# Optimization experiments

Hardware: AMD Instinct MI355X
Metric: run time of the kernel (lower is better)

The kernel has to match this reference:

```python
import jax, jax.numpy as jnp
import numpy as np

def setup_inputs() -> dict:
    key = jax.random.key(0)
    kS, kD = jax.random.split(key)
    B, Ls, Ld, d = 8, 2048, 2048, 1024
    S = jax.random.normal(kS, (B, Ls, d), dtype=jnp.float32)
    D = jax.random.normal(kD, (B, Ld, d), dtype=jnp.float32)
    return {"S": S, "D": D}

def reference(S, D):
    # scores_D: [B, Ld, Ls] = D @ S^T ; scores_S: [B, Ls, Ld] = S @ D^T
    attn_D = jax.nn.softmax(jnp.einsum('bld,bmd->blm', D, S), axis=-1)
    attn_S = jax.nn.softmax(jnp.einsum('bmd,bld->bml', S, D), axis=-1)
    co_D = D + jnp.einsum('blm,bmd->bld', attn_D, S)
    co_S = S + jnp.einsum('bml,bld->bmd', attn_S, D)
    return (co_D, co_S)
```

## Files before the change

kernel.cpp:

```cpp
#include <hip/hip_runtime.h>

typedef __attribute__((ext_vector_type(8))) _Float16 f16x8;
typedef __attribute__((ext_vector_type(16))) float f32x16;

#define B_    8
#define LSEQ  2048
#define DIM   1024
#define QBLK  64
#define KBLK  128
#define NKB   (LSEQ / KBLK)
#define NBAND 8
#define SHIFT 104.0f

#define TILE_US   16384
#define KIMG_US   ((size_t)2 * 8 * 16 * 8 * TILE_US)
#define WS_NEED   ((size_t)2 * KIMG_US * 2)
#define WS_NEW    ((size_t)3 * KIMG_US * 2)

static __device__ __forceinline__ unsigned pk2(float a, float b) {
    return __builtin_bit_cast(unsigned, __builtin_amdgcn_cvt_pkrtz(a, b));
}

#define VMCNT(n) asm volatile("s_waitcnt vmcnt(" #n ")" ::: "memory")
#define LGKM0()  asm volatile("s_waitcnt lgkmcnt(0)" ::: "memory")
#define BAR()    do { asm volatile("" ::: "memory"); __builtin_amdgcn_s_barrier(); \
                      asm volatile("" ::: "memory"); } while (0)

static __device__ __forceinline__ void gll16(const void* g, void* l) {
    __builtin_amdgcn_global_load_lds(
        (const __attribute__((address_space(1))) void*)g,
        (__attribute__((address_space(3))) void*)l, 16, 0, 0);
}

static __device__ __forceinline__ void issue32(const unsigned short* gt, unsigned short* lb, int w, int lane) {
    #pragma unroll
    for (int j = 0; j < 4; ++j) {
        const int off = (w * 4 + j) * 1024;
        gll16((const char*)gt + off + lane * 16, (char*)lb + off);
    }
}
static __device__ __forceinline__ void issue16(const unsigned short* gt, unsigned short* lb, int w, int lane) {
    #pragma unroll
    for (int j = 0; j < 2; ++j) {
        const int off = (w * 2 + j) * 1024;
        gll16((const char*)gt + off + lane * 16, (char*)lb + off);
    }
}

__global__ __launch_bounds__(256)
void prepass(const float* __restrict__ Sp, const float* __restrict__ Dp,
             unsigned short* __restrict__ Kimg, unsigned short* __restrict__ Vimg)
{
    const int blk = blockIdx.x;
    const int dc = blk & 7;
    const int kb = (blk >> 3) & 15;
    const int b  = (blk >> 7) & 7;
    const int m  = blk >> 10;
    const float* src = (m ? Dp : Sp) + ((size_t)b * LSEQ + kb * 128) * DIM + dc * 128;
    unsigned short* kt = Kimg + (size_t)((((m * 8 + b) * 16 + kb) * 8) + dc) * TILE_US;
    unsigned short* vt = Vimg + (size_t)((((m * 8 + b) * 8 + dc) * 16) + kb) * TILE_US;

    __shared__ unsigned short tile[128 * 132];
    const int t = threadIdx.x;

    #pragma unroll
    for (int i = 0; i < 16; ++i) {
        const int idx = t + i * 256;
        const int r = idx >> 5;
        const int c4 = (idx & 31) << 2;
        const float4 v = *(const float4*)(src + (size_t)r * DIM + c4);
        const unsigned lo = pk2(v.x, v.y), hi2 = pk2(v.z, v.w);
        *(uint2*)(kt + r * 128 + (c4 ^ ((r & 15) << 3))) = make_uint2(lo, hi2);
        *(uint2*)(&tile[r * 132 + c4]) = make_uint2(lo, hi2);
    }
    __syncthreads();
    #pragma unroll
    for (int i = 0; i < 32; ++i) {
        const int widx = t + i * 256;
        const int dcl = widx >> 6;
        const int wk  = widx & 63;
        const unsigned a  = tile[(wk * 2) * 132 + dcl];
        const unsigned bb = tile[(wk * 2 + 1) * 132 + dcl];
        ((unsigned*)vt)[dcl * 64 + (wk ^ ((dcl & 15) << 2))] = a | (bb << 16);
    }
}

__global__ __launch_bounds__(512, 2)
void coattn_qk(const unsigned short* __restrict__ Kimg,
               unsigned short* __restrict__ scores)
{
    const int s  = blockIdx.x;
    const int b  = s & 7;
    const int qb = s >> 3;
    const int q0 = qb * QBLK;

    const unsigned short* kbase = Kimg + (size_t)(0 * 8 + b) * 16 * 8 * TILE_US;
    const unsigned short* qbase = Kimg + (size_t)(1 * 8 + b) * 16 * 8 * TILE_US
                                + (size_t)(qb >> 1) * 8 * TILE_US + (size_t)(qb & 1) * 8192;
    unsigned short* scb = scores + (size_t)b * LSEQ * LSEQ;

    __shared__ unsigned short Rr[3][16384];
    __shared__ unsigned short QR_[3][8192];

    const int t    = threadIdx.x;
    const int lane = t & 63;
    const int w    = t >> 6;
    const int l31  = lane & 31;
    const int hi   = lane >> 5;
    const int ksub = w & 3;
    const int qh   = w >> 2;

    const int krow = ksub * 32 + l31;
    const int qrow = qh * 32 + l31;
    const int kswz = (krow & 15) << 3;
    const int qswz = (qrow & 15) << 3;

    #define QK_MMA(SLOT)                                                          \
    do {                                                                          \
        const unsigned short* Kb = Rr[SLOT];                                      \
        const unsigned short* Qb = QR_[SLOT];                                     \
        __builtin_amdgcn_s_setprio(1);                                            \
        _Pragma("unroll")                                                         \
        for (int kc = 0; kc < 8; ++kc) {                                          \
            const int d0 = kc * 16 + hi * 8;                                      \
            f16x8 a  = *(const f16x8*)&Kb[krow * 128 + (d0 ^ kswz)];              \
            f16x8 bq = *(const f16x8*)&Qb[qrow * 128 + (d0 ^ qswz)];              \
            C = __builtin_amdgcn_mfma_f32_32x32x16_f16(a, bq, C, 0, 0, 0);        \
        }                                                                         \
        __builtin_amdgcn_s_setprio(0);                                            \
    } while (0)

    #pragma unroll 1
    for (int kb = 0; kb < NKB; ++kb) {
        const unsigned short* kt = kbase + (size_t)kb * 8 * TILE_US;

        f32x16 C;
        #pragma unroll
        for (int r = 0; r < 16; ++r) C[r] = 0.0f;

        BAR();
        issue32(kt + 0 * TILE_US, Rr[0], w, lane);
        issue16(qbase + 0 * TILE_US, QR_[0], w, lane);
        issue32(kt + 1 * TILE_US, Rr[1], w, lane);
        issue16(qbase + 1 * TILE_US, QR_[1], w, lane);
        VMCNT(6);
        BAR();

        issue32(kt + 2 * TILE_US, Rr[2], w, lane);
        issue16(qbase + 2 * TILE_US, QR_[2], w, lane);
        VMCNT(6);
        QK_MMA(0);

        BAR();
        issue32(kt + 3 * TILE_US, Rr[0], w, lane);
        issue16(qbase + 3 * TILE_US, QR_[0], w, lane);
        VMCNT(6);
        QK_MMA(1);

        BAR();
        issue32(kt + 4 * TILE_US, Rr[1], w, lane);
        issue16(qbase + 4 * TILE_US, QR_[1], w, lane);
        VMCNT(6);
        QK_MMA(2);

        BAR();
        issue32(kt + 5 * TILE_US, Rr[2], w, lane);
        issue16(qbase + 5 * TILE_US, QR_[2], w, lane);
        VMCNT(6);
        QK_MMA(0);

        BAR();
        issue32(kt + 6 * TILE_US, Rr[0], w, lane);
        issue16(qbase + 6 * TILE_US, QR_[0], w, lane);
        VMCNT(6);
        QK_MMA(1);

        BAR();
        issue32(kt + 7 * TILE_US, Rr[1], w, lane);
        issue16(qbase + 7 * TILE_US, QR_[1], w, lane);
        VMCNT(6);
        QK_MMA(2);

        BAR();
        VMCNT(0);
        QK_MMA(0);

        BAR();
        QK_MMA(1);

        {
            const size_t rowoff = (size_t)(q0 + 32 * qh + l31) * LSEQ + kb * 128 + 32 * ksub;
            #pragma unroll
            for (int rp = 0; rp < 8; ++rp) {
                const int r  = rp * 2;
                const int kk = (r & 3) + 8 * (r >> 2) + 4 * hi;
                *(unsigned*)(scb + rowoff + kk) = pk2(C[r] - SHIFT, C[r + 1] - SHIFT);
            }
        }
    }
}

__global__ __launch_bounds__(512, 2)
void coattn_pv(const float* __restrict__ Sp, const float* __restrict__ Dp,
               float* __restrict__ outp,
               const unsigned short* __restrict__ Vimg,
               const unsigned short* __restrict__ scores,
               const int trans)
{
    const int s  = blockIdx.x;
    const int b  = s & 7;
    const int qb = s >> 3;
    const int q0 = qb * QBLK;

    const float* Qg = (trans ? Sp : Dp) + (size_t)b * LSEQ * DIM;
    float* Og = outp + (size_t)(trans ? 1 : 0) * ((size_t)B_ * LSEQ * DIM) + (size_t)b * LSEQ * DIM;
    const unsigned short* vbase = Vimg + (size_t)((trans ? 1 : 0) * 8 + b) * 8 * 16 * TILE_US;
    const unsigned short* scb = scores + (size_t)b * LSEQ * LSEQ;

    __shared__ unsigned short Rr[3][16384];
    __shared__ unsigned short Pst[QBLK * 128];
    __shared__ float alf[QBLK];

    const int t    = threadIdx.x;
    const int lane = t & 63;
    const int w    = t >> 6;
    const int l31  = lane & 31;
    const int hi   = lane >> 5;
    const int ksub = w & 3;
    const int qh   = w >> 2;

    const int qrow = qh * 32 + l31;
    const int qswz = (qrow & 15);
    const int dcl  = ksub * 32 + l31;
    const int vswz = (dcl & 15) << 3;

    const int srow = t >> 3;
    const int soct = t & 7;

    f32x16 O[NBAND];
    #pragma unroll
    for (int i = 0; i < NBAND; ++i)
        #pragma unroll
        for (int r = 0; r < 16; ++r) O[i][r] = 0.0f;

    float m_run = -INFINITY, l_run = 0.0f;

    #define PV_MMA(BAND, SLOT)                                                    \
    do {                                                                          \
        const unsigned short* Vb = Rr[SLOT];                                      \
        __builtin_amdgcn_s_setprio(1);                                            \
        _Pragma("unroll")                                                         \
        for (int kc = 0; kc < 8; ++kc) {                                          \
            const int kk0 = kc * 16 + hi * 8;                                     \
            f16x8 vb = *(const f16x8*)&Vb[dcl * 128 + (kk0 ^ vswz)];              \
            O[BAND] = __builtin_amdgcn_mfma_f32_32x32x16_f16(pa[kc], vb, O[BAND], 0, 0, 0); \
        }                                                                         \
        __builtin_amdgcn_s_setprio(0);                                            \
    } while (0)

    #define ISSUE_V(VI, SL) issue32(vbase + (size_t)((VI) * 16 + kb) * TILE_US, Rr[SL], w, lane)

    #pragma unroll 1
    for (int kb = 0; kb < NKB; ++kb) {
        BAR();

        if (!trans) {
            #pragma unroll
            for (int j = 0; j < 2; ++j) {
                const int G = (w * 2 + j) * 64 + lane;
                const int qq = G >> 4, gg = G & 15;
                const unsigned short* src = scb + (size_t)(q0 + qq) * LSEQ + kb * 128
                                          + ((gg ^ (qq & 15)) << 3);
                gll16(src, (char*)Pst + G * 16);
            }
        }
        ISSUE_V(0, 0);
        ISSUE_V(1, 1);
        if (!trans) { VMCNT(8); }
        BAR();

        if (trans) {
            const int drp = t >> 3;
            const int oct = t & 7;
            const unsigned short* s0 = scb + (size_t)(kb * 128 + 2 * drp) * LSEQ + q0 + oct * 8;
            const uint4 a  = *(const uint4*)s0;
            const uint4 bb = *(const uint4*)(s0 + LSEQ);
            const unsigned short* au = (const unsigned short*)&a;
            const unsigned short* bu = (const unsigned short*)&bb;
            #pragma unroll
            for (int i = 0; i < 8; ++i) {
                const int sc = oct * 8 + i;
                const unsigned v = (unsigned)au[i] | ((unsigned)bu[i] << 16);
                *(unsigned*)((char*)Pst + sc * 256 + ((((drp >> 2) ^ (sc & 15)) << 4) + (drp & 3) * 4)) = v;
            }
            LGKM0(); BAR();
        }

        {
            const int g0 = soct * 2;
            char* a0 = (char*)Pst + srow * 256 + (((g0    ) ^ (srow & 15)) << 4);
            char* a1 = (char*)Pst + srow * 256 + (((g0 + 1) ^ (srow & 15)) << 4);
            f16x8 v0 = *(const f16x8*)a0;
            f16x8 v1 = *(const f16x8*)a1;
            float sv[16];
            #pragma unroll
            for (int i = 0; i < 8; ++i) { sv[i] = (float)v0[i]; sv[8 + i] = (float)v1[i]; }
            float rm = sv[0];
            #pragma unroll
            for (int i = 1; i < 16; ++i) rm = fmaxf(rm, sv[i]);
            rm = fmaxf(rm, __shfl_xor(rm, 1));
            rm = fmaxf(rm, __shfl_xor(rm, 2));
            rm = fmaxf(rm, __shfl_xor(rm, 4));
            const float mn = fmaxf(m_run, rm);
            const float al = __expf(m_run - mn);
            float ps = 0.0f;
            #pragma unroll
            for (int i = 0; i < 16; ++i) { sv[i] = __expf(sv[i] - mn); ps += sv[i]; }
            ps += __shfl_xor(ps, 1);
            ps += __shfl_xor(ps, 2);
            ps += __shfl_xor(ps, 4);
            l_run = l_run * al + ps;
            m_run = mn;
            uint4 o0, o1;
            o0.x = pk2(sv[0], sv[1]);  o0.y = pk2(sv[2], sv[3]);
            o0.z = pk2(sv[4], sv[5]);  o0.w = pk2(sv[6], sv[7]);
            o1.x = pk2(sv[8], sv[9]);  o1.y = pk2(sv[10], sv[11]);
            o1.z = pk2(sv[12], sv[13]); o1.w = pk2(sv[14], sv[15]);
            *(uint4*)a0 = o0;
            *(uint4*)a1 = o1;
            if (soct == 0) alf[srow] = al;
        }
        LGKM0(); VMCNT(4); BAR();

        f16x8 pa[8];
        #pragma unroll
        for (int kc = 0; kc < 8; ++kc)
            pa[kc] = *(const f16x8*)((char*)Pst + qrow * 256 + (((2 * kc + hi) ^ qswz) << 4));
        {
            float alr[16];
            #pragma unroll
            for (int r = 0; r < 16; ++r)
                alr[r] = alf[qh * 32 + (r & 3) + 8 * (r >> 2) + 4 * hi];
            #pragma unroll
            for (int i = 0; i < NBAND; ++i)
                #pragma unroll
                for (int r = 0; r < 16; ++r) O[i][r] *= alr[r];
        }

        ISSUE_V(2, 2); VMCNT(4); PV_MMA(0, 0); BAR();
        ISSUE_V(3, 0); VMCNT(4); PV_MMA(1, 1); BAR();
        ISSUE_V(4, 1); VMCNT(4); PV_MMA(2, 2); BAR();
        ISSUE_V(5, 2); VMCNT(4); PV_MMA(3, 0); BAR();
        ISSUE_V(6, 0); VMCNT(4); PV_MMA(4, 1); BAR();
        ISSUE_V(7, 1); VMCNT(4); PV_MMA(5, 2); BAR();
        VMCNT(0);      PV_MMA(6, 0); BAR();
        PV_MMA(7, 1);
    }

    __syncthreads();
    if (soct == 0) alf[srow] = 1.0f / l_run;
    __syncthreads();
    #pragma unroll
    for (int r = 0; r < 16; ++r) {
        const int qr = qh * 32 + (r & 3) + 8 * (r >> 2) + 4 * hi;
        const float il = alf[qr];
        const size_t rowoff = (size_t)(q0 + qr) * DIM;
        #pragma unroll
        for (int band = 0; band < NBAND; ++band) {
            const int dcol = band * 128 + ksub * 32 + l31;
            Og[rowoff + dcol] = Qg[rowoff + dcol] + O[band][r] * il;
        }
    }
    #undef PV_MMA
    #undef ISSUE_V
    #undef QK_MMA
}

__global__ __launch_bounds__(512, 2)
void coattn_main(const float* __restrict__ Sp, const float* __restrict__ Dp,
                 float* __restrict__ outp,
                 const unsigned short* __restrict__ Kimg,
                 const unsigned short* __restrict__ Vimg)
{
    const int s   = blockIdx.x;
    const int g   = (s & 7) | ((s >> 8) << 3);
    const int qb  = (s >> 3) & 31;
    const int dir = g >> 3;
    const int b   = g & 7;
    const int mat_k = dir;
    const int mat_q = 1 - dir;

    const float* Qg = (dir ? Sp : Dp) + (size_t)b * LSEQ * DIM;
    float* Og = outp + (size_t)dir * ((size_t)B_ * LSEQ * DIM) + (size_t)b * LSEQ * DIM;
    const int q0 = qb * QBLK;

    const unsigned short* kbase = Kimg + (size_t)(mat_k * 8 + b) * 16 * 8 * TILE_US;
    const unsigned short* qbase = Kimg + (size_t)(mat_q * 8 + b) * 16 * 8 * TILE_US
                                + (size_t)(qb >> 1) * 8 * TILE_US + (size_t)(qb & 1) * 8192;
    const unsigned short* vbase = Vimg + (size_t)(mat_k * 8 + b) * 8 * 16 * TILE_US;

    __shared__ unsigned short Rr[3][16384];
    __shared__ unsigned short QR_[3][8192];
    __shared__ float redmax[2][4][32];
    __shared__ float redsum[2][4][32];
    __shared__ float alf[QBLK];

    const int t    = threadIdx.x;
    const int lane = t & 63;
    const int w    = t >> 6;
    const int l31  = lane & 31;
    const int hi   = lane >> 5;
    const int ksub = w & 3;
    const int qh   = w >> 2;

    const int krow = ksub * 32 + l31;
    const int qrow = qh * 32 + l31;
    const int kswz = (krow & 15) << 3;
    const int qswz = (qrow & 15) << 3;
    const int dcl  = ksub * 32 + l31;
    const int vswz = (dcl & 15) << 3;

    unsigned short* Plds = QR_[0];

    f32x16 O[NBAND];
    #pragma unroll
    for (int i = 0; i < NBAND; ++i)
        #pragma unroll
        for (int r = 0; r < 16; ++r) O[i][r] = 0.0f;

    float m_run = -INFINITY, l_run = 0.0f;

    #define QK_MMA(SLOT)                                                          \
    do {                                                                          \
        const unsigned short* Kb = Rr[SLOT];                                      \
        const unsigned short* Qb = QR_[SLOT];                                     \
        __builtin_amdgcn_s_setprio(1);                                            \
        _Pragma("unroll")                                                         \
        for (int kc = 0; kc < 8; ++kc) {                                          \
            const int d0 = kc * 16 + hi * 8;                                      \
            f16x8 a  = *(const f16x8*)&Kb[krow * 128 + (d0 ^ kswz)];              \
            f16x8 bq = *(const f16x8*)&Qb[qrow * 128 + (d0 ^ qswz)];              \
            C = __builtin_amdgcn_mfma_f32_32x32x16_f16(a, bq, C, 0, 0, 0);        \
        }                                                                         \
        __builtin_amdgcn_s_setprio(0);                                            \
    } while (0)

    #define PV_MMA(BAND, SLOT)                                                    \
    do {                                                                          \
        const unsigned short* Vb = Rr[SLOT];                                      \
        __builtin_amdgcn_s_setprio(1);                                            \
        _Pragma("unroll")                                                         \
        for (int kc = 0; kc < 8; ++kc) {                                          \
            const int kk0 = kc * 16 + hi * 8;                                     \
            f16x8 vb = *(const f16x8*)&Vb[dcl * 128 + (kk0 ^ vswz)];              \
            O[BAND] = __builtin_amdgcn_mfma_f32_32x32x16_f16(pa[kc], vb, O[BAND], 0, 0, 0); \
        }                                                                         \
        __builtin_amdgcn_s_setprio(0);                                            \
    } while (0)

    #pragma unroll 1
    for (int kb = 0; kb < NKB; ++kb) {
        const unsigned short* kt = kbase + (size_t)kb * 8 * TILE_US;

        f32x16 C;
        #pragma unroll
        for (int r = 0; r < 16; ++r) C[r] = 0.0f;

        BAR();
        issue32(kt + 0 * TILE_US, Rr[0], w, lane);
        issue16(qbase + 0 * TILE_US, QR_[0], w, lane);
        issue32(kt + 1 * TILE_US, Rr[1], w, lane);
        issue16(qbase + 1 * TILE_US, QR_[1], w, lane);
        VMCNT(6);
        BAR();

        issue32(kt + 2 * TILE_US, Rr[2], w, lane);
        issue16(qbase + 2 * TILE_US, QR_[2], w, lane);
        VMCNT(6);
        QK_MMA(0);

        BAR();
        issue32(kt + 3 * TILE_US, Rr[0], w, lane);
        issue16(qbase + 3 * TILE_US, QR_[0], w, lane);
        VMCNT(6);
        QK_MMA(1);

        BAR();
        issue32(kt + 4 * TILE_US, Rr[1], w, lane);
        issue16(qbase + 4 * TILE_US, QR_[1], w, lane);
        VMCNT(6);
        QK_MMA(2);

        BAR();
        issue32(kt + 5 * TILE_US, Rr[2], w, lane);
        issue16(qbase + 5 * TILE_US, QR_[2], w, lane);
        VMCNT(6);
        QK_MMA(0);

        BAR();
        issue32(kt + 6 * TILE_US, Rr[0], w, lane);
        issue16(qbase + 6 * TILE_US, QR_[0], w, lane);
        VMCNT(6);
        QK_MMA(1);

        BAR();
        issue32(kt + 7 * TILE_US, Rr[1], w, lane);
        issue16(qbase + 7 * TILE_US, QR_[1], w, lane);
        VMCNT(6);
        QK_MMA(2);

        BAR();
        issue32(vbase + (size_t)(0 * 16 + kb) * TILE_US, Rr[2], w, lane);
        VMCNT(4);
        QK_MMA(0);

        BAR();
        issue32(vbase + (size_t)(1 * 16 + kb) * TILE_US, Rr[0], w, lane);
        VMCNT(4);
        QK_MMA(1);

        float rm = -INFINITY;
        #pragma unroll
        for (int r = 0; r < 16; ++r) rm = fmaxf(rm, C[r]);
        rm = fmaxf(rm, __shfl_xor(rm, 32));
        if (lane < 32) redmax[qh][ksub][l31] = rm;
        __syncthreads();

        const float bm = fmaxf(fmaxf(redmax[qh][0][l31], redmax[qh][1][l31]),
                               fmaxf(redmax[qh][2][l31], redmax[qh][3][l31]));
        const float mn = fmaxf(m_run, bm);
        const float al = __expf(m_run - mn);
        float p[16];
        float ps = 0.0f;
        #pragma unroll
        for (int r = 0; r < 16; ++r) { p[r] = __expf(C[r] - mn); ps += p[r]; }
        ps += __shfl_xor(ps, 32);
        if (lane < 32) {
            redsum[qh][ksub][l31] = ps;
            if (ksub == 0) alf[qh * 32 + l31] = al;
        }
        {
            #pragma unroll
            for (int rp = 0; rp < 8; ++rp) {
                const int r  = rp * 2;
                const int kk = ksub * 32 + (r & 3) + 8 * (r >> 2) + 4 * hi;
                *(unsigned*)&Plds[qrow * KBLK + (kk ^ qswz)] = pk2(p[r], p[r + 1]);
            }
        }
        __syncthreads();

        const float bs = redsum[qh][0][l31] + redsum[qh][1][l31] +
                         redsum[qh][2][l31] + redsum[qh][3][l31];
        l_run = l_run * al + bs;
        m_run = mn;

        float alr[16];
        #pragma unroll
        for (int r = 0; r < 16; ++r)
            alr[r] = alf[qh * 32 + (r & 3) + 8 * (r >> 2) + 4 * hi];
        #pragma unroll
        for (int i = 0; i < NBAND; ++i)
            #pragma unroll
            for (int r = 0; r < 16; ++r) O[i][r] *= alr[r];

        f16x8 pa[8];
        #pragma unroll
        for (int kc = 0; kc < 8; ++kc) {
            const int kk0 = kc * 16 + hi * 8;
            pa[kc] = *(const f16x8*)&Plds[qrow * KBLK + (kk0 ^ qswz)];
        }

        issue32(vbase + (size_t)(2 * 16 + kb) * TILE_US, Rr[1], w, lane);
        VMCNT(4);
        PV_MMA(0, 2);

        BAR();
        issue32(vbase + (size_t)(3 * 16 + kb) * TILE_US, Rr[2], w, lane);
        VMCNT(4);
        PV_MMA(1, 0);

        BAR();
        issue32(vbase + (size_t)(4 * 16 + kb) * TILE_US, Rr[0], w, lane);
        VMCNT(4);
        PV_MMA(2, 1);

        BAR();
        issue32(vbase + (size_t)(5 * 16 + kb) * TILE_US, Rr[1], w, lane);
        VMCNT(4);
        PV_MMA(3, 2);

        BAR();
        issue32(vbase + (size_t)(6 * 16 + kb) * TILE_US, Rr[2], w, lane);
        VMCNT(4);
        PV_MMA(4, 0);

        BAR();
        issue32(vbase + (size_t)(7 * 16 + kb) * TILE_US, Rr[0], w, lane);
        VMCNT(4);
        PV_MMA(5, 1);

        BAR();
        PV_MMA(6, 2);

        BAR();
        VMCNT(0);
        PV_MMA(7, 0);
    }

    __syncthreads();
    if (lane < 32 && ksub == 0) alf[qh * 32 + l31] = 1.0f / l_run;
    __syncthreads();
    #pragma unroll
    for (int r = 0; r < 16; ++r) {
        const int qr = qh * 32 + (r & 3) + 8 * (r >> 2) + 4 * hi;
        const float il = alf[qr];
        const size_t rowoff = (size_t)(q0 + qr) * DIM;
        #pragma unroll
        for (int band = 0; band < NBAND; ++band) {
            const int dcol = band * 128 + ksub * 32 + l31;
            Og[rowoff + dcol] = Qg[rowoff + dcol] + O[band][r] * il;
        }
    }
    #undef QK_MMA
    #undef PV_MMA
}

#define NDC   8

__global__ __launch_bounds__(512, 2)
void coattn_fb(const float* __restrict__ Sp, const float* __restrict__ Dp,
               float* __restrict__ outp)
{
    const int s   = blockIdx.x;
    const int g   = (s & 7) | ((s >> 8) << 3);
    const int qb  = (s >> 3) & 31;
    const int dir = g >> 3;
    const int b   = g & 7;

    const float* Qg = (dir ? Sp : Dp) + (size_t)b * LSEQ * DIM;
    const float* Kg = (dir ? Dp : Sp) + (size_t)b * LSEQ * DIM;
    float* Og = outp + (size_t)dir * ((size_t)B_ * LSEQ * DIM) + (size_t)b * LSEQ * DIM;
    const int q0 = qb * QBLK;

    __shared__ unsigned short Klds[KBLK * 128];
    __shared__ unsigned short Qlds[QBLK * 128];
    __shared__ unsigned short Plds[QBLK * KBLK];
    __shared__ unsigned short Vlds[128 * KBLK];
    __shared__ float redmax[2][4][32];
    __shared__ float redsum[2][4][32];
    __shared__ float alf[QBLK];

    const int t    = threadIdx.x;
    const int lane = t & 63;
    const int w    = t >> 6;
    const int l31  = lane & 31;
    const int hi   = lane >> 5;
    const int ksub = w & 3;
    const int qh   = w >> 2;

    f32x16 O[NBAND];
    #pragma unroll
    for (int i = 0; i < NBAND; ++i)
        #pragma unroll
        for (int r = 0; r < 16; ++r) O[i][r] = 0.0f;

    float m_run = -INFINITY, l_run = 0.0f;

    const int srow = t >> 4;
    const int fcol = (t & 15) << 2;
    const int vmm  = t & 31;
    const int vkp0 = t >> 5;

    const int krow = ksub * 32 + l31;
    const int qrow = qh * 32 + l31;

    for (int kb = 0; kb < NKB; ++kb) {
        const int k0g = kb * KBLK;
        f32x16 C;
        #pragma unroll
        for (int r = 0; r < 16; ++r) C[r] = 0.0f;

        float4 kreg[8], qreg[4];
        #pragma unroll
        for (int pass = 0; pass < 4; ++pass)
            #pragma unroll
            for (int h = 0; h < 2; ++h)
                kreg[pass * 2 + h] = *(const float4*)(Kg + (size_t)(k0g + pass * 32 + srow) * DIM + fcol + h * 64);
        #pragma unroll
        for (int pass = 0; pass < 2; ++pass)
            #pragma unroll
            for (int h = 0; h < 2; ++h)
                qreg[pass * 2 + h] = *(const float4*)(Qg + (size_t)(q0 + pass * 32 + srow) * DIM + fcol + h * 64);

        #pragma unroll 1
        for (int dc = 0; dc < NDC; ++dc) {
            __syncthreads();
            #pragma unroll
            for (int pass = 0; pass < 4; ++pass)
                #pragma unroll
                for (int h = 0; h < 2; ++h) {
                    const int row = pass * 32 + srow;
                    const int d   = fcol + h * 64;
                    const float4 v = kreg[pass * 2 + h];
                    *(uint2*)&Klds[row * 128 + (d ^ ((row & 7) << 3))] =
                        make_uint2(pk2(v.x, v.y), pk2(v.z, v.w));
                }
            #pragma unroll
            for (int pass = 0; pass < 2; ++pass)
                #pragma unroll
                for (int h = 0; h < 2; ++h) {
                    const int row = pass * 32 + srow;
                    const int d   = fcol + h * 64;
                    const float4 v = qreg[pass * 2 + h];
                    *(uint2*)&Qlds[row * 128 + (d ^ ((row & 7) << 3))] =
                        make_uint2(pk2(v.x, v.y), pk2(v.z, v.w));
                }
            __syncthreads();
            if (dc + 1 < NDC) {
                const int dbase = (dc + 1) * 128;
                #pragma unroll
                for (int pass = 0; pass < 4; ++pass)
                    #pragma unroll
                    for (int h = 0; h < 2; ++h)
                        kreg[pass * 2 + h] = *(const float4*)(Kg + (size_t)(k0g + pass * 32 + srow) * DIM + dbase + fcol + h * 64);
                #pragma unroll
                for (int pass = 0; pass < 2; ++pass)
                    #pragma unroll
                    for (int h = 0; h < 2; ++h)
                        qreg[pass * 2 + h] = *(const float4*)(Qg + (size_t)(q0 + pass * 32 + srow) * DIM + dbase + fcol + h * 64);
            }
            #pragma unroll
            for (int kc = 0; kc < 8; ++kc) {
                const int d0 = kc * 16 + hi * 8;
                f16x8 a  = *(const f16x8*)&Klds[krow * 128 + (d0 ^ ((krow & 7) << 3))];
                f16x8 bq = *(const f16x8*)&Qlds[qrow * 128 + (d0 ^ ((qrow & 7) << 3))];
                C = __builtin_amdgcn_mfma_f32_32x32x16_f16(a, bq, C, 0, 0, 0);
            }
        }

        float rm = -INFINITY;
        #pragma unroll
        for (int r = 0; r < 16; ++r) rm = fmaxf(rm, C[r]);
        rm = fmaxf(rm, __shfl_xor(rm, 32));
        if (lane < 32) redmax[qh][ksub][l31] = rm;
        __syncthreads();

        const float bm = fmaxf(fmaxf(redmax[qh][0][l31], redmax[qh][1][l31]),
                               fmaxf(redmax[qh][2][l31], redmax[qh][3][l31]));
        const float mn = fmaxf(m_run, bm);
        const float al = __expf(m_run - mn);
        float p[16];
        float ps = 0.0f;
        #pragma unroll
        for (int r = 0; r < 16; ++r) { p[r] = __expf(C[r] - mn); ps += p[r]; }
        ps += __shfl_xor(ps, 32);
        if (lane < 32) {
            redsum[qh][ksub][l31] = ps;
            if (ksub == 0) alf[qh * 32 + l31] = al;
        }
        {
            #pragma unroll
            for (int rp = 0; rp < 8; ++rp) {
                const int r  = rp * 2;
                const int kk = ksub * 32 + (r & 3) + 8 * (r >> 2) + 4 * hi;
                *(unsigned*)&Plds[qrow * KBLK + (kk ^ ((qrow & 7) << 3))] = pk2(p[r], p[r + 1]);
            }
        }
        __syncthreads();

        const float bs = redsum[qh][0][l31] + redsum[qh][1][l31] +
                         redsum[qh][2][l31] + redsum[qh][3][l31];
        l_run = l_run * al + bs;
        m_run = mn;

        float alr[16];
        #pragma unroll
        for (int r = 0; r < 16; ++r)
            alr[r] = alf[qh * 32 + (r & 3) + 8 * (r >> 2) + 4 * hi];
        #pragma unroll
        for (int i = 0; i < NBAND; ++i)
            #pragma unroll
            for (int r = 0; r < 16; ++r) O[i][r] *= alr[r];

        f16x8 pa[8];
        #pragma unroll
        for (int kc = 0; kc < 8; ++kc) {
            const int kk0 = kc * 16 + hi * 8;
            pa[kc] = *(const f16x8*)&Plds[qrow * KBLK + (kk0 ^ ((qrow & 7) << 3))];
        }

        float4 v0s[4], v1s[4];
        #pragma unroll
        for (int pass = 0; pass < 4; ++pass) {
            const int kp = pass * 16 + vkp0;
            v0s[pass] = *(const float4*)(Kg + (size_t)(k0g + 2 * kp) * DIM + vmm * 4);
            v1s[pass] = *(const float4*)(Kg + (size_t)(k0g + 2 * kp + 1) * DIM + vmm * 4);
        }

        #pragma unroll
        for (int band = 0; band < NBAND; ++band) {
            __syncthreads();
            #pragma unroll
            for (int pass = 0; pass < 4; ++pass) {
                const int kp = pass * 16 + vkp0;
                const float* a0 = (const float*)&v0s[pass];
                const float* a1 = (const float*)&v1s[pass];
                #pragma unroll
                for (int j = 0; j < 4; ++j) {
                    const int dclw = vmm * 4 + j;
                    *(unsigned*)&Vlds[dclw * KBLK + ((2 * kp) ^ ((dclw & 7) << 3))] = pk2(a0[j], a1[j]);
                }
            }
            __syncthreads();
            if (band + 1 < NBAND) {
                const int cb = (band + 1) * 128;
                #pragma unroll
                for (int pass = 0; pass < 4; ++pass) {
                    const int kp = pass * 16 + vkp0;
                    v0s[pass] = *(const float4*)(Kg + (size_t)(k0g + 2 * kp) * DIM + cb + vmm * 4);
                    v1s[pass] = *(const float4*)(Kg + (size_t)(k0g + 2 * kp + 1) * DIM + cb + vmm * 4);
                }
            }
            const int dclr = ksub * 32 + l31;
            const int sw  = (dclr & 7) << 3;
            #pragma unroll
            for (int kc = 0; kc < 8; ++kc) {
                const int kk0 = kc * 16 + hi * 8;
                f16x8 vb = *(const f16x8*)&Vlds[dclr * KBLK + (kk0 ^ sw)];
                O[band] = __builtin_amdgcn_mfma_f32_32x32x16_f16(pa[kc], vb, O[band], 0, 0, 0);
            }
        }
    }

    if (lane < 32 && ksub == 0) alf[qh * 32 + l31] = 1.0f / l_run;
    __syncthreads();
    #pragma unroll
    for (int r = 0; r < 16; ++r) {
        const int qr = qh * 32 + (r & 3) + 8 * (r >> 2) + 4 * hi;
        const float il = alf[qr];
        const size_t rowoff = (size_t)(q0 + qr) * DIM;
        #pragma unroll
        for (int band = 0; band < NBAND; ++band) {
            const int dcol = band * 128 + ksub * 32 + l31;
            Og[rowoff + dcol] = Qg[rowoff + dcol] + O[band][r] * il;
        }
    }
}

extern "C" void kernel_launch(void* const* d_in, const int* in_sizes, int n_in,
                              void* d_out, int out_size, void* d_ws, size_t ws_size,
                              hipStream_t stream) {
    const float* S = (const float*)d_in[0];
    const float* D = (const float*)d_in[1];
    float* out = (float*)d_out;
    if (ws_size >= WS_NEW) {
        unsigned short* Kimg   = (unsigned short*)d_ws;
        unsigned short* Vimg   = Kimg + KIMG_US;
        unsigned short* scores = Vimg + KIMG_US;
        prepass<<<dim3(2048, 1, 1), dim3(256, 1, 1), 0, stream>>>(S, D, Kimg, Vimg);
        coattn_qk<<<dim3(256, 1, 1), dim3(512, 1, 1), 0, stream>>>(Kimg, scores);
        coattn_pv<<<dim3(256, 1, 1), dim3(512, 1, 1), 0, stream>>>(S, D, out, Vimg, scores, 0);
        coattn_pv<<<dim3(256, 1, 1), dim3(512, 1, 1), 0, stream>>>(S, D, out, Vimg, scores, 1);
    } else if (ws_size >= WS_NEED) {
        unsigned short* Kimg = (unsigned short*)d_ws;
        unsigned short* Vimg = Kimg + KIMG_US;
        prepass<<<dim3(2048, 1, 1), dim3(256, 1, 1), 0, stream>>>(S, D, Kimg, Vimg);
        coattn_main<<<dim3(512, 1, 1), dim3(512, 1, 1), 0, stream>>>(S, D, out, Kimg, Vimg);
    } else {
        coattn_fb<<<dim3(512, 1, 1), dim3(512, 1, 1), 0, stream>>>(S, D, out);
    }
}
```

Baseline: 566.3 us.

## Pipeline QK tile loads across key blocks and merge both PV launches

The QK kernel's per-key-block prologue and drain are replaced by a single continuous triple-buffered stream over all 128 tiles, so loads for the next key block overlap the tail MMAs of the current one. The two PV launches (one per direction) are merged into one 512-block grid, with the direction taken from the block index. This removes pipeline bubbles and one launch and its tail, at the cost of slightly more index arithmetic and a rolled inner loop.

```diff
diff --git a/kernel.cpp b/kernel.cpp
--- a/kernel.cpp
+++ b/kernel.cpp
@@ -25,6 +25,8 @@
 #define LGKM0()  asm volatile("s_waitcnt lgkmcnt(0)" ::: "memory")
 #define BAR()    do { asm volatile("" ::: "memory"); __builtin_amdgcn_s_barrier(); \
                       asm volatile("" ::: "memory"); } while (0)
+
+static __device__ __forceinline__ int s3(int x) { return x >= 3 ? x - 3 : x; }
 
 static __device__ __forceinline__ void gll16(const void* g, void* l) {
     __builtin_amdgcn_global_load_lds(
@@ -130,63 +132,36 @@
         __builtin_amdgcn_s_setprio(0);                                            \
     } while (0)
 
+    issue32(kbase + 0 * TILE_US, Rr[0], w, lane);
+    issue16(qbase + 0 * TILE_US, QR_[0], w, lane);
+    issue32(kbase + 1 * TILE_US, Rr[1], w, lane);
+    issue16(qbase + 1 * TILE_US, QR_[1], w, lane);
+    VMCNT(6);
+    BAR();
+
+    int sl = 0;
+
     #pragma unroll 1
     for (int kb = 0; kb < NKB; ++kb) {
-        const unsigned short* kt = kbase + (size_t)kb * 8 * TILE_US;
-
         f32x16 C;
         #pragma unroll
         for (int r = 0; r < 16; ++r) C[r] = 0.0f;
 
-        BAR();
-        issue32(kt + 0 * TILE_US, Rr[0], w, lane);
-        issue16(qbase + 0 * TILE_US, QR_[0], w, lane);
-        issue32(kt + 1 * TILE_US, Rr[1], w, lane);
-        issue16(qbase + 1 * TILE_US, QR_[1], w, lane);
-        VMCNT(6);
-        BAR();
-
-        issue32(kt + 2 * TILE_US, Rr[2], w, lane);
-        issue16(qbase + 2 * TILE_US, QR_[2], w, lane);
-        VMCNT(6);
-        QK_MMA(0);
-
-        BAR();
-        issue32(kt + 3 * TILE_US, Rr[0], w, lane);
-        issue16(qbase + 3 * TILE_US, QR_[0], w, lane);
-        VMCNT(6);
-        QK_MMA(1);
-
-        BAR();
-        issue32(kt + 4 * TILE_US, Rr[1], w, lane);
-        issue16(qbase + 4 * TILE_US, QR_[1], w, lane);
-        VMCNT(6);
-        QK_MMA(2);
-
-        BAR();
-        issue32(kt + 5 * TILE_US, Rr[2], w, lane);
-        issue16(qbase + 5 * TILE_US, QR_[2], w, lane);
-        VMCNT(6);
-        QK_MMA(0);
-
-        BAR();
-        issue32(kt + 6 * TILE_US, Rr[0], w, lane);
-        issue16(qbase + 6 * TILE_US, QR_[0], w, lane);
-        VMCNT(6);
-        QK_MMA(1);
-
-        BAR();
-        issue32(kt + 7 * TILE_US, Rr[1], w, lane);
-        issue16(qbase + 7 * TILE_US, QR_[1], w, lane);
-        VMCNT(6);
-        QK_MMA(2);
-
-        BAR();
-        VMCNT(0);
-        QK_MMA(0);
-
-        BAR();
-        QK_MMA(1);
+        #pragma unroll 1
+        for (int c = 0; c < 8; ++c) {
+            const int i  = kb * 8 + c;
+            const int ni = i + 2;
+            if (ni < 128) {
+                issue32(kbase + (size_t)ni * TILE_US, Rr[s3(sl + 2)], w, lane);
+                issue16(qbase + (size_t)(ni & 7) * TILE_US, QR_[s3(sl + 2)], w, lane);
+                VMCNT(6);
+            } else if (i == 126) {
+                VMCNT(0);
+            }
+            QK_MMA(sl);
+            BAR();
+            sl = s3(sl + 1);
+        }
 
         {
             const size_t rowoff = (size_t)(q0 + 32 * qh + l31) * LSEQ + kb * 128 + 32 * ksub;
@@ -198,18 +173,19 @@
             }
         }
     }
+    #undef QK_MMA
 }
 
 __global__ __launch_bounds__(512, 2)
 void coattn_pv(const float* __restrict__ Sp, const float* __restrict__ Dp,
                float* __restrict__ outp,
                const unsigned short* __restrict__ Vimg,
-               const unsigned short* __restrict__ scores,
-               const int trans)
+               const unsigned short* __restrict__ scores)
 {
-    const int s  = blockIdx.x;
+    const int s     = blockIdx.x;
+    const int trans = s >> 8;
     const int b  = s & 7;
-    const int qb = s >> 3;
+    const int qb = (s >> 3) & 31;
     const int q0 = qb * QBLK;
 
     const float* Qg = (trans ? Sp : Dp) + (size_t)b * LSEQ * DIM;
@@ -373,7 +349,6 @@
     }
     #undef PV_MMA
     #undef ISSUE_V
-    #undef QK_MMA
 }
 
 __global__ __launch_bounds__(512, 2)
@@ -859,8 +834,7 @@
         unsigned short* scores = Vimg + KIMG_US;
         prepass<<<dim3(2048, 1, 1), dim3(256, 1, 1), 0, stream>>>(S, D, Kimg, Vimg);
         coattn_qk<<<dim3(256, 1, 1), dim3(512, 1, 1), 0, stream>>>(Kimg, scores);
-        coattn_pv<<<dim3(256, 1, 1), dim3(512, 1, 1), 0, stream>>>(S, D, out, Vimg, scores, 0);
-        coattn_pv<<<dim3(256, 1, 1), dim3(512, 1, 1), 0, stream>>>(S, D, out, Vimg, scores, 1);
+        coattn_pv<<<dim3(512, 1, 1), dim3(512, 1, 1), 0, stream>>>(S, D, out, Vimg, scores);
     } else if (ws_size >= WS_NEED) {
         unsigned short* Kimg = (unsigned short*)d_ws;
         unsigned short* Vimg = Kimg + KIMG_US;
```

After: 593.1 us. 1.05x slower.
